# Kernel optimization log

Hardware: AMD Instinct MI355X
Metric: run time of the kernel (lower is better)

The kernel has to match this reference:

```python
import jax, jax.numpy as jnp
import numpy as np

NT, NX = 64, 64
N_HALF = NT * NX // 2  # 2048 sites per checkerboard half

# mask[:, ::2] = False -> True at odd-x columns (the 'A' half)
_mask = np.ones((NT, NX), dtype=bool)
_mask[:, ::2] = False
IDX_A = jnp.asarray(np.where(_mask.reshape(-1))[0])   # [N_HALF]
IDX_B = jnp.asarray(np.where(~_mask.reshape(-1))[0])  # [N_HALF]


def setup_inputs() -> dict:
    key = jax.random.key(0)
    k0, k1, k2, k3, k4 = jax.random.split(key, 5)
    B = 4096
    scale = 1.0 / np.sqrt(N_HALF)
    return {
        "input_phi": jax.random.normal(k0, (B, NT, NX), dtype=jnp.float32),
        "W_s": jax.random.normal(k1, (N_HALF, N_HALF), dtype=jnp.float32) * scale,
        "b_s": jnp.zeros((N_HALF,), dtype=jnp.float32),
        "W_t": jax.random.normal(k2, (N_HALF, N_HALF), dtype=jnp.float32) * scale,
        "b_t": jnp.zeros((N_HALF,), dtype=jnp.float32),
    }


def _coupling(A, B, W_s, b_s, W_t, b_t):
    # Affine coupling: A' = A * exp(s(B)) + t(B); logDetJ = sum(s(B))
    s = jnp.tanh(B @ W_s.T + b_s)   # [batch, N_HALF]
    t = B @ W_t.T + b_t             # [batch, N_HALF]
    return A * jnp.exp(s) + t, jnp.sum(s, axis=-1)


def reference(input_phi, W_s, b_s, W_t, b_t):
    lead = input_phi.shape[:-2]
    phi = input_phi.reshape(*lead, NT * NX)
    A = phi[..., IDX_A]  # [batch, N_HALF]
    B = phi[..., IDX_B]
    A, logDetJc1 = _coupling(A, B, W_s, b_s, W_t, b_t)
    B, logDetJc2 = _coupling(B, A, W_s, b_s, W_t, b_t)
    out = jnp.zeros_like(phi).at[..., IDX_A].set(A).at[..., IDX_B].set(B)
    return out.reshape(*lead, NT, NX), logDetJc1 + logDetJc2
```

## Files before the change

### kernel.cpp

```cpp
#include <hip/hip_runtime.h>
#include <stdint.h>

#define BATCH 4096
#define NTX   4096
#define NH    2048
#define KDIM  2048

#define BM 256
#define BN 128
#define BK 64
#define THREADS 512
#define NITER (KDIM / BK)

#define A_OFF 0
#define S_OFF 16384
#define T_OFF 24576
#define BUF_E 32768

typedef __bf16 bf16x8 __attribute__((ext_vector_type(8)));
typedef float  f32x4  __attribute__((ext_vector_type(4)));

__device__ __forceinline__ unsigned short f2bf(float f) {
    union { float f; unsigned u; } v; v.f = f;
    unsigned u = v.u;
    unsigned r = u + 0x7fffu + ((u >> 16) & 1u);
    return (unsigned short)(r >> 16);
}

__device__ __forceinline__ float fast_tanh(float x) {
    float e = __expf(x + x);
    return 1.f - 2.f / (e + 1.f);
}

typedef __attribute__((address_space(1))) void gvoid;
typedef __attribute__((address_space(3))) void lvoid;

__device__ __forceinline__ void async16(const unsigned short* g, unsigned short* l) {
    __builtin_amdgcn_global_load_lds((gvoid*)(void*)g, (lvoid*)l, 16, 0, 0);
}

__device__ __forceinline__ int roff(int R, int c) {
    return R * BK + (((c) + (R & 7)) & 7) * 8;
}

__global__ void prep(const float* __restrict__ phi,
                     const float* __restrict__ Wsf,
                     const float* __restrict__ Wtf,
                     unsigned short* __restrict__ Bbf,
                     unsigned short* __restrict__ Wsb,
                     unsigned short* __restrict__ Wtb,
                     float* __restrict__ out)
{
    const int tid    = blockIdx.x * blockDim.x + threadIdx.x;
    const int stride = gridDim.x * blockDim.x;

    const float4* p4 = (const float4*)phi;
    for (int i = tid; i < (BATCH * NH / 4); i += stride) {
        float4 u = p4[2 * i], v = p4[2 * i + 1];
        uint2 o;
        o.x = (unsigned)f2bf(u.x) | ((unsigned)f2bf(u.z) << 16);
        o.y = (unsigned)f2bf(v.x) | ((unsigned)f2bf(v.z) << 16);
        ((uint2*)Bbf)[i] = o;
    }

    const float4* ws4 = (const float4*)Wsf;
    const float4* wt4 = (const float4*)Wtf;
    for (int i = tid; i < (NH * KDIM / 8); i += stride) {
        float4 u = ws4[2 * i], v = ws4[2 * i + 1];
        uint4 o;
        o.x = (unsigned)f2bf(u.x) | ((unsigned)f2bf(u.y) << 16);
        o.y = (unsigned)f2bf(u.z) | ((unsigned)f2bf(u.w) << 16);
        o.z = (unsigned)f2bf(v.x) | ((unsigned)f2bf(v.y) << 16);
        o.w = (unsigned)f2bf(v.z) | ((unsigned)f2bf(v.w) << 16);
        ((uint4*)Wsb)[i] = o;
        u = wt4[2 * i]; v = wt4[2 * i + 1];
        o.x = (unsigned)f2bf(u.x) | ((unsigned)f2bf(u.y) << 16);
        o.y = (unsigned)f2bf(u.z) | ((unsigned)f2bf(u.w) << 16);
        o.z = (unsigned)f2bf(v.x) | ((unsigned)f2bf(v.y) << 16);
        o.w = (unsigned)f2bf(v.z) | ((unsigned)f2bf(v.w) << 16);
        ((uint4*)Wtb)[i] = o;
    }

    for (int i = tid; i < BATCH; i += stride) out[(size_t)BATCH * NTX + i] = 0.f;
}

__global__ __launch_bounds__(THREADS, 2) void coupling_gemm(
    const unsigned short* __restrict__ X,
    const unsigned short* __restrict__ Wsb,
    const unsigned short* __restrict__ Wtb,
    const float* __restrict__ bs,
    const float* __restrict__ bt,
    const float* __restrict__ phi,
    float* __restrict__ out,
    unsigned short* __restrict__ Xout,
    int parity)
{
    __shared__ unsigned short lds[2][BUF_E];

    const int tid = threadIdx.x;
    const int m0 = blockIdx.x * BM;
    const int n0 = blockIdx.y * BN;

    f32x4 acc_s[4][4], acc_t[4][4];
    const f32x4 zf = {0.f, 0.f, 0.f, 0.f};
#pragma unroll
    for (int i = 0; i < 4; i++)
#pragma unroll
        for (int j = 0; j < 4; j++) { acc_s[i][j] = zf; acc_t[i][j] = zf; }

    const int srow = tid >> 3;
    const int cg   = ((tid & 7) - (srow & 7)) & 7;
    const unsigned short* Ag = X   + (size_t)(m0 + srow) * KDIM + cg * 8;
    const unsigned short* Sg = Wsb + (size_t)(n0 + srow) * KDIM + cg * 8;
    const unsigned short* Tg = Wtb + (size_t)(n0 + srow) * KDIM + cg * 8;
    const size_t r64  = (size_t)64  * KDIM;
    const size_t r128 = (size_t)128 * KDIM;
    const int lw = tid * 8;

    const int wave = tid >> 6;
    const int lane = tid & 63;
    const int wm = (wave >> 1) * 64;
    const int wn = (wave & 1) * 64;
    const int lrow = lane & 15;
    const int kc   = lane >> 4;

    int aO[4], sO[4], tO[4];
#pragma unroll
    for (int i = 0; i < 4; i++) {
        aO[i] = A_OFF + roff(wm + i * 16 + lrow, kc);
        sO[i] = S_OFF + roff(wn + i * 16 + lrow, kc);
        tO[i] = T_OFF + roff(wn + i * 16 + lrow, kc);
    }

    {
        unsigned short* b = &lds[0][0];
        async16(Ag,              b + A_OFF + lw);
        async16(Ag + r64,        b + A_OFF + 4096 + lw);
        async16(Ag + r128,       b + A_OFF + 8192 + lw);
        async16(Ag + r128 + r64, b + A_OFF + 12288 + lw);
        async16(Sg,              b + S_OFF + lw);
        async16(Sg + r64,        b + S_OFF + 4096 + lw);
        async16(Tg,              b + T_OFF + lw);
        async16(Tg + r64,        b + T_OFF + 4096 + lw);
    }
    asm volatile("s_waitcnt vmcnt(2)" ::: "memory");
    __builtin_amdgcn_s_barrier();

    for (int t = 0; t < NITER; ++t) {
        unsigned short* bc = &lds[t & 1][0];
        unsigned short* bx = &lds[(t & 1) ^ 1][0];
        const int k0n = (((t + 1) < NITER) ? (t + 1) : 0) * BK;

        bf16x8 a0[4], a1[4], f[4];

#pragma unroll
        for (int i = 0; i < 4; i++) {
            a0[i] = *(const bf16x8*)(bc + aO[i]);
            f[i]  = *(const bf16x8*)(bc + sO[i]);
        }
        async16(Ag + k0n,       bx + A_OFF + lw);
        async16(Ag + k0n + r64, bx + A_OFF + 4096 + lw);
        __builtin_amdgcn_s_barrier();
        __builtin_amdgcn_s_setprio(1);
#pragma unroll
        for (int mi = 0; mi < 4; mi++)
#pragma unroll
            for (int ni = 0; ni < 4; ni++)
                acc_s[mi][ni] = __builtin_amdgcn_mfma_f32_16x16x32_bf16(
                    a0[mi], f[ni], acc_s[mi][ni], 0, 0, 0);
        __builtin_amdgcn_s_setprio(0);
        __builtin_amdgcn_s_barrier();

#pragma unroll
        for (int i = 0; i < 4; i++) {
            a1[i] = *(const bf16x8*)(bc + (aO[i] ^ 32));
            f[i]  = *(const bf16x8*)(bc + (sO[i] ^ 32));
        }
        async16(Ag + k0n + r128,       bx + A_OFF + 8192 + lw);
        async16(Ag + k0n + r128 + r64, bx + A_OFF + 12288 + lw);
        __builtin_amdgcn_s_barrier();
        __builtin_amdgcn_s_setprio(1);
#pragma unroll
        for (int mi = 0; mi < 4; mi++)
#pragma unroll
            for (int ni = 0; ni < 4; ni++)
                acc_s[mi][ni] = __builtin_amdgcn_mfma_f32_16x16x32_bf16(
                    a1[mi], f[ni], acc_s[mi][ni], 0, 0, 0);
        __builtin_amdgcn_s_setprio(0);
        asm volatile("s_waitcnt vmcnt(4)" ::: "memory");
        __builtin_amdgcn_s_barrier();

#pragma unroll
        for (int i = 0; i < 4; i++)
            f[i] = *(const bf16x8*)(bc + tO[i]);
        async16(Sg + k0n,       bx + S_OFF + lw);
        async16(Sg + k0n + r64, bx + S_OFF + 4096 + lw);
        __builtin_amdgcn_s_barrier();
        __builtin_amdgcn_s_setprio(1);
#pragma unroll
        for (int mi = 0; mi < 4; mi++)
#pragma unroll
            for (int ni = 0; ni < 4; ni++)
                acc_t[mi][ni] = __builtin_amdgcn_mfma_f32_16x16x32_bf16(
                    a0[mi], f[ni], acc_t[mi][ni], 0, 0, 0);
        __builtin_amdgcn_s_setprio(0);
        __builtin_amdgcn_s_barrier();

#pragma unroll
        for (int i = 0; i < 4; i++)
            f[i] = *(const bf16x8*)(bc + (tO[i] ^ 32));
        async16(Tg + k0n,       bx + T_OFF + lw);
        async16(Tg + k0n + r64, bx + T_OFF + 4096 + lw);
        __builtin_amdgcn_s_barrier();
        __builtin_amdgcn_s_setprio(1);
#pragma unroll
        for (int mi = 0; mi < 4; mi++)
#pragma unroll
            for (int ni = 0; ni < 4; ni++)
                acc_t[mi][ni] = __builtin_amdgcn_mfma_f32_16x16x32_bf16(
                    a1[mi], f[ni], acc_t[mi][ni], 0, 0, 0);
        __builtin_amdgcn_s_setprio(0);
        asm volatile("s_waitcnt vmcnt(2)" ::: "memory");
        __builtin_amdgcn_s_barrier();
    }

    float* ldslot = out + (size_t)BATCH * NTX;
#pragma unroll
    for (int mi = 0; mi < 4; mi++) {
#pragma unroll
        for (int r = 0; r < 4; r++) {
            const int brow = m0 + wm + mi * 16 + (lane >> 4) * 4 + r;
            float ssum = 0.f;
#pragma unroll
            for (int ni = 0; ni < 4; ni++) {
                const int n = n0 + wn + ni * 16 + lrow;
                float s  = fast_tanh(acc_s[mi][ni][r] + bs[n]);
                float tv = acc_t[mi][ni][r] + bt[n];
                const size_t oidx = (size_t)brow * NTX + 2 * n + parity;
                float val = fmaf(phi[oidx], __expf(s), tv);
                out[oidx] = val;
                if (Xout) Xout[(size_t)brow * NH + n] = f2bf(val);
                ssum += s;
            }
            ssum += __shfl_xor(ssum, 1);
            ssum += __shfl_xor(ssum, 2);
            ssum += __shfl_xor(ssum, 4);
            ssum += __shfl_xor(ssum, 8);
            if (lrow == 0) atomicAdd(ldslot + brow, ssum);
        }
    }
}

extern "C" void kernel_launch(void* const* d_in, const int* in_sizes, int n_in,
                              void* d_out, int out_size, void* d_ws, size_t ws_size,
                              hipStream_t stream) {
    const float* phi = (const float*)d_in[0];
    const float* Wsf = (const float*)d_in[1];
    const float* bs  = (const float*)d_in[2];
    const float* Wtf = (const float*)d_in[3];
    const float* bt  = (const float*)d_in[4];
    float* out = (float*)d_out;

    char* ws = (char*)d_ws;
    unsigned short* Bbf  = (unsigned short*)(ws);
    unsigned short* Apbf = (unsigned short*)(ws + 16777216);
    unsigned short* Wsb  = (unsigned short*)(ws + 33554432);
    unsigned short* Wtb  = (unsigned short*)(ws + 41943040);

    prep<<<1024, 256, 0, stream>>>(phi, Wsf, Wtf, Bbf, Wsb, Wtb, out);

    coupling_gemm<<<dim3(16, 16), THREADS, 0, stream>>>(
        Bbf, Wsb, Wtb, bs, bt, phi, out, Apbf, 1);

    coupling_gemm<<<dim3(16, 16), THREADS, 0, stream>>>(
        Apbf, Wsb, Wtb, bs, bt, phi, out, nullptr, 0);
}
```

Baseline: 315.2 us.

## Pre-split phi into packed halves and write interleaved output with paired stores

The prep kernel now de-interleaves phi into contiguous fp32 A and B buffers in workspace. The first GEMM reads its packed A half and writes its result to a packed buffer instead of strided output. The second GEMM then writes both halves together as float2 stores into the interleaved output. This replaces stride-2 scalar epilogue loads and stores with contiguous access, at the cost of extra workspace traffic in prep. The change also sets launch bounds occupancy to 1 and doubles the prep grid, and the packed path only runs if the workspace is at least 144MB.

```diff
diff --git a/kernel.cpp b/kernel.cpp
--- a/kernel.cpp
+++ b/kernel.cpp
@@ -49,7 +49,9 @@
                      unsigned short* __restrict__ Bbf,
                      unsigned short* __restrict__ Wsb,
                      unsigned short* __restrict__ Wtb,
-                     float* __restrict__ out)
+                     float* __restrict__ out,
+                     float* __restrict__ phiA,
+                     float* __restrict__ phiB)
 {
     const int tid    = blockIdx.x * blockDim.x + threadIdx.x;
     const int stride = gridDim.x * blockDim.x;
@@ -61,6 +63,12 @@
         o.x = (unsigned)f2bf(u.x) | ((unsigned)f2bf(u.z) << 16);
         o.y = (unsigned)f2bf(v.x) | ((unsigned)f2bf(v.z) << 16);
         ((uint2*)Bbf)[i] = o;
+        if (phiA) {
+            float4 a; a.x = u.y; a.y = u.w; a.z = v.y; a.w = v.w;
+            ((float4*)phiA)[i] = a;
+            float4 b; b.x = u.x; b.y = u.z; b.z = v.x; b.w = v.z;
+            ((float4*)phiB)[i] = b;
+        }
     }
 
     const float4* ws4 = (const float4*)Wsf;
@@ -84,7 +92,7 @@
     for (int i = tid; i < BATCH; i += stride) out[(size_t)BATCH * NTX + i] = 0.f;
 }
 
-__global__ __launch_bounds__(THREADS, 2) void coupling_gemm(
+__global__ __launch_bounds__(THREADS, 1) void coupling_gemm(
     const unsigned short* __restrict__ X,
     const unsigned short* __restrict__ Wsb,
     const unsigned short* __restrict__ Wtb,
@@ -93,7 +101,11 @@
     const float* __restrict__ phi,
     float* __restrict__ out,
     unsigned short* __restrict__ Xout,
-    int parity)
+    int parity,
+    const float* __restrict__ pin_packed,
+    float* __restrict__ apack_w,
+    const float* __restrict__ apack_r,
+    int mode)
 {
     __shared__ unsigned short lds[2][BUF_E];
 
@@ -146,9 +158,10 @@
     asm volatile("s_waitcnt vmcnt(2)" ::: "memory");
     __builtin_amdgcn_s_barrier();
 
-    for (int t = 0; t < NITER; ++t) {
-        unsigned short* bc = &lds[t & 1][0];
-        unsigned short* bx = &lds[(t & 1) ^ 1][0];
+    for (int t = 0; t < NITER; t++) {
+        const int cur = t & 1;
+        unsigned short* bc = &lds[cur][0];
+        unsigned short* bx = &lds[cur ^ 1][0];
         const int k0n = (((t + 1) < NITER) ? (t + 1) : 0) * BK;
 
         bf16x8 a0[4], a1[4], f[4];
@@ -236,10 +249,20 @@
                 const int n = n0 + wn + ni * 16 + lrow;
                 float s  = fast_tanh(acc_s[mi][ni][r] + bs[n]);
                 float tv = acc_t[mi][ni][r] + bt[n];
-                const size_t oidx = (size_t)brow * NTX + 2 * n + parity;
-                float val = fmaf(phi[oidx], __expf(s), tv);
-                out[oidx] = val;
+                float pin;
+                if (mode != 0) pin = pin_packed[(size_t)brow * NH + n];
+                else           pin = phi[(size_t)brow * NTX + 2 * n + parity];
+                float val = fmaf(pin, __expf(s), tv);
                 if (Xout) Xout[(size_t)brow * NH + n] = f2bf(val);
+                if (mode == 1) {
+                    apack_w[(size_t)brow * NH + n] = val;
+                } else if (mode == 2) {
+                    float2 o2; o2.x = val;
+                    o2.y = apack_r[(size_t)brow * NH + n];
+                    ((float2*)(out + (size_t)brow * NTX))[n] = o2;
+                } else {
+                    out[(size_t)brow * NTX + 2 * n + parity] = val;
+                }
                 ssum += s;
             }
             ssum += __shfl_xor(ssum, 1);
@@ -267,11 +290,18 @@
     unsigned short* Wsb  = (unsigned short*)(ws + 33554432);
     unsigned short* Wtb  = (unsigned short*)(ws + 41943040);
 
-    prep<<<1024, 256, 0, stream>>>(phi, Wsf, Wtf, Bbf, Wsb, Wtb, out);
+    const int packed = (ws_size >= (size_t)144 * 1024 * 1024) ? 1 : 0;
+    float* phiA  = packed ? (float*)(ws + (size_t) 48 * 1024 * 1024) : nullptr;
+    float* phiB  = packed ? (float*)(ws + (size_t) 80 * 1024 * 1024) : nullptr;
+    float* Apack = packed ? (float*)(ws + (size_t)112 * 1024 * 1024) : nullptr;
+
+    prep<<<2048, 256, 0, stream>>>(phi, Wsf, Wtf, Bbf, Wsb, Wtb, out, phiA, phiB);
 
     coupling_gemm<<<dim3(16, 16), THREADS, 0, stream>>>(
-        Bbf, Wsb, Wtb, bs, bt, phi, out, Apbf, 1);
+        Bbf, Wsb, Wtb, bs, bt, phi, out, Apbf, 1,
+        phiA, Apack, nullptr, packed ? 1 : 0);
 
     coupling_gemm<<<dim3(16, 16), THREADS, 0, stream>>>(
-        Apbf, Wsb, Wtb, bs, bt, phi, out, nullptr, 0);
-}
+        Apbf, Wsb, Wtb, bs, bt, phi, out, nullptr, 0,
+        phiB, nullptr, Apack, packed ? 2 : 0);
+}
```

Result: slower. 326.8 us (+3.6%).

## Restructure GEMM main loop into two phases with batched prefetch

Applied to the files above, without the earlier changes.

The k-loop goes from four LDS-read/MFMA phases, each issuing part of the next tile's async loads, to two phases. All A and S fragments for both k-halves load up front, all eight async global-to-LDS copies for the next tile are issued at once, and the loop waits for vmcnt(0) at its end. sched_barrier hints pin instruction ordering. The aim is fewer barriers and longer MFMA runs, at the cost of more live registers and less staggered load overlap. The prep kernel grid is also doubled.

```diff
diff --git a/kernel.cpp b/kernel.cpp
--- a/kernel.cpp
+++ b/kernel.cpp
@@ -143,84 +143,67 @@
         async16(Tg,              b + T_OFF + lw);
         async16(Tg + r64,        b + T_OFF + 4096 + lw);
     }
-    asm volatile("s_waitcnt vmcnt(2)" ::: "memory");
+    asm volatile("s_waitcnt vmcnt(0)" ::: "memory");
     __builtin_amdgcn_s_barrier();
 
-    for (int t = 0; t < NITER; ++t) {
-        unsigned short* bc = &lds[t & 1][0];
-        unsigned short* bx = &lds[(t & 1) ^ 1][0];
+    for (int t = 0; t < NITER; t++) {
+        const int cur = t & 1;
+        unsigned short* bc = &lds[cur][0];
+        unsigned short* bx = &lds[cur ^ 1][0];
         const int k0n = (((t + 1) < NITER) ? (t + 1) : 0) * BK;
 
-        bf16x8 a0[4], a1[4], f[4];
+        bf16x8 a0[4], a1[4], f0[4], f1[4];
 
 #pragma unroll
         for (int i = 0; i < 4; i++) {
             a0[i] = *(const bf16x8*)(bc + aO[i]);
-            f[i]  = *(const bf16x8*)(bc + sO[i]);
+            a1[i] = *(const bf16x8*)(bc + (aO[i] ^ 32));
+            f0[i] = *(const bf16x8*)(bc + sO[i]);
+            f1[i] = *(const bf16x8*)(bc + (sO[i] ^ 32));
         }
-        async16(Ag + k0n,       bx + A_OFF + lw);
-        async16(Ag + k0n + r64, bx + A_OFF + 4096 + lw);
-        __builtin_amdgcn_s_barrier();
-        __builtin_amdgcn_s_setprio(1);
-#pragma unroll
-        for (int mi = 0; mi < 4; mi++)
-#pragma unroll
-            for (int ni = 0; ni < 4; ni++)
-                acc_s[mi][ni] = __builtin_amdgcn_mfma_f32_16x16x32_bf16(
-                    a0[mi], f[ni], acc_s[mi][ni], 0, 0, 0);
-        __builtin_amdgcn_s_setprio(0);
-        __builtin_amdgcn_s_barrier();
-
-#pragma unroll
-        for (int i = 0; i < 4; i++) {
-            a1[i] = *(const bf16x8*)(bc + (aO[i] ^ 32));
-            f[i]  = *(const bf16x8*)(bc + (sO[i] ^ 32));
-        }
+        async16(Ag + k0n,              bx + A_OFF + lw);
+        async16(Ag + k0n + r64,        bx + A_OFF + 4096 + lw);
         async16(Ag + k0n + r128,       bx + A_OFF + 8192 + lw);
         async16(Ag + k0n + r128 + r64, bx + A_OFF + 12288 + lw);
+        async16(Sg + k0n,              bx + S_OFF + lw);
+        async16(Sg + k0n + r64,        bx + S_OFF + 4096 + lw);
+        async16(Tg + k0n,              bx + T_OFF + lw);
+        async16(Tg + k0n + r64,        bx + T_OFF + 4096 + lw);
+        __builtin_amdgcn_sched_barrier(0);
         __builtin_amdgcn_s_barrier();
         __builtin_amdgcn_s_setprio(1);
 #pragma unroll
         for (int mi = 0; mi < 4; mi++)
 #pragma unroll
-            for (int ni = 0; ni < 4; ni++)
+            for (int ni = 0; ni < 4; ni++) {
                 acc_s[mi][ni] = __builtin_amdgcn_mfma_f32_16x16x32_bf16(
-                    a1[mi], f[ni], acc_s[mi][ni], 0, 0, 0);
+                    a0[mi], f0[ni], acc_s[mi][ni], 0, 0, 0);
+                acc_s[mi][ni] = __builtin_amdgcn_mfma_f32_16x16x32_bf16(
+                    a1[mi], f1[ni], acc_s[mi][ni], 0, 0, 0);
+            }
         __builtin_amdgcn_s_setprio(0);
-        asm volatile("s_waitcnt vmcnt(4)" ::: "memory");
-        __builtin_amdgcn_s_barrier();
-
-#pragma unroll
-        for (int i = 0; i < 4; i++)
-            f[i] = *(const bf16x8*)(bc + tO[i]);
-        async16(Sg + k0n,       bx + S_OFF + lw);
-        async16(Sg + k0n + r64, bx + S_OFF + 4096 + lw);
+        __builtin_amdgcn_s_barrier();
+
+#pragma unroll
+        for (int i = 0; i < 4; i++) {
+            f0[i] = *(const bf16x8*)(bc + tO[i]);
+            f1[i] = *(const bf16x8*)(bc + (tO[i] ^ 32));
+        }
+        __builtin_amdgcn_sched_barrier(0);
         __builtin_amdgcn_s_barrier();
         __builtin_amdgcn_s_setprio(1);
 #pragma unroll
         for (int mi = 0; mi < 4; mi++)
 #pragma unroll
-            for (int ni = 0; ni < 4; ni++)
+            for (int ni = 0; ni < 4; ni++) {
                 acc_t[mi][ni] = __builtin_amdgcn_mfma_f32_16x16x32_bf16(
-                    a0[mi], f[ni], acc_t[mi][ni], 0, 0, 0);
+                    a0[mi], f0[ni], acc_t[mi][ni], 0, 0, 0);
+                acc_t[mi][ni] = __builtin_amdgcn_mfma_f32_16x16x32_bf16(
+                    a1[mi], f1[ni], acc_t[mi][ni], 0, 0, 0);
+            }
         __builtin_amdgcn_s_setprio(0);
-        __builtin_amdgcn_s_barrier();
-
-#pragma unroll
-        for (int i = 0; i < 4; i++)
-            f[i] = *(const bf16x8*)(bc + (tO[i] ^ 32));
-        async16(Tg + k0n,       bx + T_OFF + lw);
-        async16(Tg + k0n + r64, bx + T_OFF + 4096 + lw);
-        __builtin_amdgcn_s_barrier();
-        __builtin_amdgcn_s_setprio(1);
-#pragma unroll
-        for (int mi = 0; mi < 4; mi++)
-#pragma unroll
-            for (int ni = 0; ni < 4; ni++)
-                acc_t[mi][ni] = __builtin_amdgcn_mfma_f32_16x16x32_bf16(
-                    a1[mi], f[ni], acc_t[mi][ni], 0, 0, 0);
-        __builtin_amdgcn_s_setprio(0);
-        asm volatile("s_waitcnt vmcnt(2)" ::: "memory");
+        asm volatile("s_waitcnt vmcnt(0)" ::: "memory");
+        __builtin_amdgcn_sched_barrier(0);
         __builtin_amdgcn_s_barrier();
     }
 
@@ -267,7 +250,7 @@
     unsigned short* Wsb  = (unsigned short*)(ws + 33554432);
     unsigned short* Wtb  = (unsigned short*)(ws + 41943040);
 
-    prep<<<1024, 256, 0, stream>>>(phi, Wsf, Wtf, Bbf, Wsb, Wtb, out);
+    prep<<<2048, 256, 0, stream>>>(phi, Wsf, Wtf, Bbf, Wsb, Wtb, out);
 
     coupling_gemm<<<dim3(16, 16), THREADS, 0, stream>>>(
         Bbf, Wsb, Wtb, bs, bt, phi, out, Apbf, 1);
```

New measurement: 320.2 us. About the same (+1.6%).
